# Optimization experiments

Hardware: AMD Instinct MI355X
Metric: run time of the kernel (lower is better)

Reference implementation:

```python
import math
import jax, jax.numpy as jnp
import numpy as np

B, S, D, H, DH = 2, 2048, 2048, 16, 128  # batch, seq (= n_ctx), d_model, n_heads, d_head


def _alibi_slopes(n):
    def pow2(m):
        start = 2 ** (-2 ** (-(math.log2(m) - 3)))
        return [start * start ** i for i in range(m)]
    if math.log2(n).is_integer():
        return pow2(n)
    c = 2 ** math.floor(math.log2(n))
    return pow2(c) + _alibi_slopes(2 * c)[0::2][: n - c]


def _alibi_mask(n_heads, q_len, kv_len):
    # faithful to _gen_alibi_mask: causal -inf upper triangle + slope * key_position
    slopes = jnp.asarray(np.array(_alibi_slopes(n_heads), dtype=np.float32))  # [H]
    bias = slopes[:, None, None] * jnp.arange(kv_len, dtype=jnp.float32)[None, None, :]  # [H,1,kv]
    i = jnp.arange(q_len)[:, None]
    j = jnp.arange(kv_len)[None, :]
    causal = jnp.where(j > i, -jnp.inf, 0.0).astype(jnp.float32)  # [q,kv] (q_len == kv_len here)
    return causal[None, :, :] + bias  # [H,q,kv]


def setup_inputs() -> dict:
    key = jax.random.key(0)
    k1, k2, k3, k4, k5 = jax.random.split(key, 5)
    scale = 1.0 / math.sqrt(D)
    return {
        "resid_pre": jax.random.normal(k1, (B, S, D), dtype=jnp.float32),
        "Wq": jax.random.normal(k2, (H * DH, D), dtype=jnp.float32) * scale,
        "Wk": jax.random.normal(k3, (H * DH, D), dtype=jnp.float32) * scale,
        "Wv": jax.random.normal(k4, (H * DH, D), dtype=jnp.float32) * scale,
        "Wo": jax.random.normal(k5, (D, H * DH), dtype=jnp.float32) * scale,
    }


def reference(resid_pre, Wq, Wk, Wv, Wo):
    b, s, d = resid_pre.shape
    # nn.Linear(no bias): y = x @ W^T ; view to [b, s, H, DH]
    q = (resid_pre @ Wq.T).reshape(b, s, H, DH)
    k = (resid_pre @ Wk.T).reshape(b, s, H, DH)
    v = (resid_pre @ Wv.T).reshape(b, s, H, DH)
    # QK^T / sqrt(d_head), clamp, add ALiBi+causal mask
    scores = jnp.einsum('bqhd,bkhd->bhqk', q, k) / math.sqrt(DH)
    scores = jnp.clip(scores, -1024.0, 1024.0)
    scores = scores + _alibi_mask(H, s, s)[None]  # broadcast over batch
    attn = jax.nn.softmax(scores.astype(jnp.float32), axis=-1).astype(q.dtype)
    z = jnp.einsum('bhqk,bkhd->bqhd', attn, v)  # [b,s,H,DH]
    # out_proj.weight [D, H*DH] reshaped to [D, H, DH]; per-head out summed over heads
    out = jnp.einsum('bqhd,ohd->bqo', z, Wo.reshape(d, H, DH))
    return out
```

## Files before the change

### kernel.cpp

```cpp
#include <hip/hip_runtime.h>
#include <hip/hip_bf16.h>

typedef __attribute__((ext_vector_type(4))) float f32x4;
typedef __attribute__((ext_vector_type(8))) short bf16x8;
typedef __attribute__((ext_vector_type(4))) short short4v;

__device__ __forceinline__ short f2bf(float f) {
  union { float f; unsigned u; } x; x.f = f;
  unsigned r = x.u + 0x7fffu + ((x.u >> 16) & 1u);
  return (short)(r >> 16);
}

__device__ __forceinline__ float fexp2(float x) {
#if __has_builtin(__builtin_amdgcn_exp2f)
  return __builtin_amdgcn_exp2f(x);
#else
  return exp2f(x);
#endif
}

#define WAITVM(n) { asm volatile("s_waitcnt vmcnt(" #n ")" ::: "memory"); __builtin_amdgcn_sched_barrier(0); }
#define BARRIER() { __builtin_amdgcn_sched_barrier(0); asm volatile("s_barrier" ::: "memory"); __builtin_amdgcn_sched_barrier(0); }
#define GLD16(g, l) __builtin_amdgcn_global_load_lds((const __attribute__((address_space(1))) void*)(g), (__attribute__((address_space(3))) void*)(l), 16, 0, 0)

#define QSC (0.08838834764831845f * 1.4426950408889634f)

__global__ __launch_bounds__(256) void cast_kernel(const float* __restrict__ in,
                                                   short* __restrict__ out, int n4) {
  int i = blockIdx.x * 256 + threadIdx.x;
  if (i < n4) {
    const float4 v = reinterpret_cast<const float4*>(in)[i];
    short4v s;
    s.x = f2bf(v.x); s.y = f2bf(v.y); s.z = f2bf(v.z); s.w = f2bf(v.w);
    reinterpret_cast<short4v*>(out)[i] = s;
  }
}

__global__ __launch_bounds__(256) void cast_w_kernel(const float* __restrict__ w0,
                                                     const float* __restrict__ w1,
                                                     const float* __restrict__ w2,
                                                     const float* __restrict__ w3,
                                                     short* __restrict__ qkv,
                                                     short* __restrict__ wo) {
  const int y = blockIdx.y;
  const float* in = (y == 0) ? w0 : (y == 1) ? w1 : (y == 2) ? w2 : w3;
  short* out = (y < 3) ? (qkv + (long)y * 4194304) : wo;
  const int i = blockIdx.x * 256 + threadIdx.x;
  const float4 v = reinterpret_cast<const float4*>(in)[i];
  short4v s;
  s.x = f2bf(v.x); s.y = f2bf(v.y); s.z = f2bf(v.z); s.w = f2bf(v.w);
  reinterpret_cast<short4v*>(out)[i] = s;
}

__global__ __launch_bounds__(512, 2) void gemm_qkv8(const short* __restrict__ A,
                                                    const short* __restrict__ W,
                                                    short* __restrict__ Qo,
                                                    short* __restrict__ Ko,
                                                    short* __restrict__ Vt) {
  __shared__ __align__(1024) char lds[131072];
  const int tid  = threadIdx.x;
  const int lane = tid & 63;
  const int w    = tid >> 6;
  const int wm   = w >> 2, wn = w & 3;
  const int l16  = lane & 15, g = lane >> 4;
  const int K    = 2048;

  int id = (int)blockIdx.x;
  id = (id & 7) * 64 + (id >> 3);
  const int mb = id & 31, nb = id >> 5;
  const long m0 = (long)mb * 128, n0 = (long)nb * 384;

  const int srow = lane >> 3;
  const int scol = ((lane & 7) ^ srow) * 8;
  const int csw  = (l16 & 7) << 4;

  f32x4 acc[4][6];
  #pragma unroll
  for (int a = 0; a < 4; a++)
    #pragma unroll
    for (int b = 0; b < 6; b++) acc[a][b] = (f32x4){0.f, 0.f, 0.f, 0.f};

  #define STAGE_A(kt, buf)                                                          \
    {                                                                               \
      const short* s0_ = A + (m0 + w * 16 + srow) * K + (kt) * 64 + scol;           \
      char* d_ = lds + (buf) * 65536 + (w * 16) * 128;                              \
      GLD16(s0_, d_);                                                               \
      GLD16(s0_ + 8LL * K, d_ + 1024);                                              \
    }
  #define STAGE_B(h, kt, buf)                                                       \
    {                                                                               \
      const short* s0_ = W + (n0 + (h) * 128 + w * 16 + srow) * K + (kt) * 64 + scol; \
      char* d_ = lds + (buf) * 65536 + 16384 + (h) * 16384 + (w * 16) * 128;        \
      GLD16(s0_, d_);                                                               \
      GLD16(s0_ + 8LL * K, d_ + 1024);                                              \
    }

  #define RDA(buf, fmL, k) (*reinterpret_cast<const bf16x8*>(                       \
      lds + (buf) * 65536 + ((wm * 64 + (fmL) * 16 + l16) * 128) +                  \
      ((((k) * 64 + g * 16)) ^ csw)))
  #define RDB(buf, h, j, k) (*reinterpret_cast<const bf16x8*>(                      \
      lds + (buf) * 65536 + 16384 + (h) * 16384 +                                   \
      ((wn * 16 + (j) * 64 + l16) * 128) + ((((k) * 64 + g * 16)) ^ csw)))

  STAGE_A(0, 0);
  STAGE_B(0, 0, 0);
  STAGE_B(1, 0, 0);
  STAGE_B(2, 0, 0);
  WAITVM(4);
  BARRIER();

  bf16x8 af[4][2], bfr[2][2];
  for (int kt = 0; kt < 32; ++kt) {
    const int cur = kt & 1, nxt = cur ^ 1;
    const int ks = (kt + 1 < 32) ? (kt + 1) : kt;

    #pragma unroll
    for (int fm = 0; fm < 4; fm++)
      #pragma unroll
      for (int k = 0; k < 2; k++) af[fm][k] = RDA(cur, fm, k);
    #pragma unroll
    for (int j = 0; j < 2; j++)
      #pragma unroll
      for (int k = 0; k < 2; k++) bfr[j][k] = RDB(cur, 0, j, k);
    STAGE_A(ks, nxt);
    STAGE_B(0, ks, nxt);
    WAITVM(6);
    BARRIER();
    __builtin_amdgcn_s_setprio(1);
    #pragma unroll
    for (int fm = 0; fm < 4; fm++)
      #pragma unroll
      for (int j = 0; j < 2; j++)
        #pragma unroll
        for (int k = 0; k < 2; k++)
          acc[fm][j] = __builtin_amdgcn_mfma_f32_16x16x32_bf16(af[fm][k], bfr[j][k], acc[fm][j], 0, 0, 0);
    __builtin_amdgcn_s_setprio(0);
    BARRIER();

    #pragma unroll
    for (int j = 0; j < 2; j++)
      #pragma unroll
      for (int k = 0; k < 2; k++) bfr[j][k] = RDB(cur, 1, j, k);
    STAGE_B(1, ks, nxt);
    WAITVM(6);
    BARRIER();
    __builtin_amdgcn_s_setprio(1);
    #pragma unroll
    for (int fm = 0; fm < 4; fm++)
      #pragma unroll
      for (int j = 0; j < 2; j++)
        #pragma unroll
        for (int k = 0; k < 2; k++)
          acc[fm][2 + j] = __builtin_amdgcn_mfma_f32_16x16x32_bf16(af[fm][k], bfr[j][k], acc[fm][2 + j], 0, 0, 0);
    __builtin_amdgcn_s_setprio(0);
    BARRIER();

    #pragma unroll
    for (int j = 0; j < 2; j++)
      #pragma unroll
      for (int k = 0; k < 2; k++) bfr[j][k] = RDB(cur, 2, j, k);
    STAGE_B(2, ks, nxt);
    WAITVM(4);
    BARRIER();
    __builtin_amdgcn_s_setprio(1);
    #pragma unroll
    for (int fm = 0; fm < 4; fm++)
      #pragma unroll
      for (int j = 0; j < 2; j++)
        #pragma unroll
        for (int k = 0; k < 2; k++)
          acc[fm][4 + j] = __builtin_amdgcn_mfma_f32_16x16x32_bf16(af[fm][k], bfr[j][k], acc[fm][4 + j], 0, 0, 0);
    __builtin_amdgcn_s_setprio(0);
    BARRIER();
  }

  #pragma unroll
  for (int fm = 0; fm < 4; fm++)
    #pragma unroll
    for (int fj = 0; fj < 6; fj++) {
      const long row0 = m0 + wm * 64 + fm * 16 + g * 4;
      const long col  = n0 + fj * 64 + wn * 16 + l16;
      if (col < 2048) {
        #pragma unroll
        for (int i = 0; i < 4; i++) Qo[(row0 + i) * 2048 + col] = f2bf(acc[fm][fj][i] * QSC);
      } else if (col < 4096) {
        #pragma unroll
        for (int i = 0; i < 4; i++) Ko[(row0 + i) * 2048 + (col - 2048)] = f2bf(acc[fm][fj][i]);
      } else {
        const long c2 = col - 4096;
        const long base = (((row0 >> 11) * 16 + (c2 >> 7)) * 128 + (c2 & 127)) * 2048 + (row0 & 2047);
        short4v pk;
        #pragma unroll
        for (int i = 0; i < 4; i++) pk[i] = f2bf(acc[fm][fj][i]);
        *reinterpret_cast<short4v*>(Vt + base) = pk;
      }
    }
  #undef STAGE_A
  #undef STAGE_B
  #undef RDA
  #undef RDB
}

template<typename CT, bool TV>
__global__ __launch_bounds__(256) void gemm_bt(const short* __restrict__ A,
                                               const short* __restrict__ B,
                                               CT* __restrict__ C,
                                               int M, int N, int K) {
  __shared__ short As[128][72];
  __shared__ short Bs[128][72];

  const int tid  = threadIdx.x;
  const int lane = tid & 63;
  const int w    = tid >> 6;
  const int l16  = lane & 15, g = lane >> 4;
  const int wr   = w >> 1, wc = w & 1;
  const long m0  = (long)blockIdx.y * 128;
  const long n0  = (long)blockIdx.x * 128;

  const f32x4 zero4 = {0.f, 0.f, 0.f, 0.f};
  f32x4 acc[4][4];
  #pragma unroll
  for (int a = 0; a < 4; a++)
    #pragma unroll
    for (int b2 = 0; b2 < 4; b2++) acc[a][b2] = zero4;

  const int srow0 = tid >> 3;
  const int scol  = (tid & 7) * 8;

  const int ktiles = K >> 6;
  for (int kt = 0; kt < ktiles; kt++) {
    const int k0 = kt << 6;
    __syncthreads();
    #pragma unroll
    for (int j = 0; j < 4; j++) {
      const int row = j * 32 + srow0;
      *reinterpret_cast<bf16x8*>(&As[row][scol]) =
          *reinterpret_cast<const bf16x8*>(A + (m0 + row) * K + k0 + scol);
      *reinterpret_cast<bf16x8*>(&Bs[row][scol]) =
          *reinterpret_cast<const bf16x8*>(B + (n0 + row) * K + k0 + scol);
    }
    __syncthreads();
    #pragma unroll
    for (int kk = 0; kk < 2; kk++) {
      bf16x8 af[4], bfr[4];
      #pragma unroll
      for (int f = 0; f < 4; f++)
        af[f] = *reinterpret_cast<const bf16x8*>(&As[wr * 64 + f * 16 + l16][kk * 32 + g * 8]);
      #pragma unroll
      for (int f = 0; f < 4; f++)
        bfr[f] = *reinterpret_cast<const bf16x8*>(&Bs[wc * 64 + f * 16 + l16][kk * 32 + g * 8]);
      #pragma unroll
      for (int fm = 0; fm < 4; fm++)
        #pragma unroll
        for (int fn = 0; fn < 4; fn++)
          acc[fm][fn] = __builtin_amdgcn_mfma_f32_16x16x32_bf16(af[fm], bfr[fn], acc[fm][fn], 0, 0, 0);
    }
  }

  #pragma unroll
  for (int fm = 0; fm < 4; fm++)
    #pragma unroll
    for (int fn = 0; fn < 4; fn++) {
      const long row0 = m0 + wr * 64 + fm * 16 + g * 4;
      const long col  = n0 + wc * 64 + fn * 16 + l16;
      if constexpr (TV) {
        const long base = (((row0 >> 11) * 16 + (col >> 7)) * 128 + (col & 127)) * 2048 + (row0 & 2047);
        short4v pk;
        #pragma unroll
        for (int i = 0; i < 4; i++) pk[i] = f2bf(acc[fm][fn][i]);
        *reinterpret_cast<short4v*>(C + base) = pk;
      } else {
        #pragma unroll
        for (int i = 0; i < 4; i++) {
          const float v = acc[fm][fn][i];
          if constexpr (sizeof(CT) == 2) C[(row0 + i) * N + col] = (CT)f2bf(v);
          else                           C[(row0 + i) * N + col] = v;
        }
      }
    }
}

__global__ __launch_bounds__(256, 3) void attn_kernel(const short* __restrict__ Q,
                                                      const short* __restrict__ K,
                                                      const short* __restrict__ Vt,
                                                      short* __restrict__ Z) {
  __shared__ short Ks[64][136];
  __shared__ short Vs[128][72];
  __shared__ short plds[4][16][72];

  const int tid  = threadIdx.x;
  const int lane = tid & 63;
  const int w    = tid >> 6;
  const int l16  = lane & 15, g = lane >> 4;

  const int bh = blockIdx.x;
  const int bx = 31 - (int)blockIdx.y;
  const int b  = bh >> 4, h = bh & 15;
  const int q0 = bx * 64;

  const float LOG2E  = 1.4426950408889634f;
  const float slope2 = exp2f(-0.5f * (float)(h + 1)) * LOG2E;
  const float CLAMP2 = 1477.3197f;

  bf16x8 qf[4];
  {
    const long qoff = ((long)(b * 2048 + q0 + w * 16 + l16)) * 2048 + h * 128;
    #pragma unroll
    for (int c = 0; c < 4; c++)
      qf[c] = *reinterpret_cast<const bf16x8*>(Q + qoff + c * 32 + g * 8);
  }

  const f32x4 zero4 = {0.f, 0.f, 0.f, 0.f};
  f32x4 zacc[8];
  #pragma unroll
  for (int s = 0; s < 8; s++) zacc[s] = zero4;
  float m2[4], li[4];
  #pragma unroll
  for (int i = 0; i < 4; i++) { m2[i] = -3e38f; li[i] = 0.f; }

  float aj[4];
  #pragma unroll
  for (int ni = 0; ni < 4; ni++) aj[ni] = slope2 * (float)(ni * 16 + l16);

  const int krow = tid >> 4, kcol = (tid & 15) * 8;
  const int vrow = tid >> 3, vcol = (tid & 7) * 8;
  const short* Kh = K + ((long)b * 2048) * 2048 + h * 128;
  const short* Vh = Vt + ((long)(b * 16 + h) * 128) * 2048;

  bf16x8 kreg[4], vreg[4];
  #pragma unroll
  for (int j = 0; j < 4; j++)
    kreg[j] = *reinterpret_cast<const bf16x8*>(Kh + (long)(j * 16 + krow) * 2048 + kcol);
  #pragma unroll
  for (int j = 0; j < 4; j++)
    vreg[j] = *reinterpret_cast<const bf16x8*>(Vh + (long)(j * 32 + vrow) * 2048 + vcol);

  const int ntiles = bx + 1;
  for (int t = 0; t < ntiles; t++) {
    const int kv0 = t * 64;
    __syncthreads();
    #pragma unroll
    for (int j = 0; j < 4; j++)
      *reinterpret_cast<bf16x8*>(&Ks[j * 16 + krow][kcol]) = kreg[j];
    #pragma unroll
    for (int j = 0; j < 4; j++)
      *reinterpret_cast<bf16x8*>(&Vs[j * 32 + vrow][vcol]) = vreg[j];
    __syncthreads();

    f32x4 sc[4];
    #pragma unroll
    for (int ni = 0; ni < 4; ni++) sc[ni] = zero4;
    #pragma unroll
    for (int ni = 0; ni < 4; ni++)
      #pragma unroll
      for (int kc = 0; kc < 4; kc++) {
        const bf16x8 kf = *reinterpret_cast<const bf16x8*>(&Ks[ni * 16 + l16][kc * 32 + g * 8]);
        sc[ni] = __builtin_amdgcn_mfma_f32_16x16x32_bf16(qf[kc], kf, sc[ni], 0, 0, 0);
      }

    if (t + 1 < ntiles) {
      const short* kb = Kh + (long)(kv0 + 64) * 2048;
      const short* vb = Vh + kv0 + 64;
      #pragma unroll
      for (int j = 0; j < 4; j++)
        kreg[j] = *reinterpret_cast<const bf16x8*>(kb + (long)(j * 16 + krow) * 2048 + kcol);
      #pragma unroll
      for (int j = 0; j < 4; j++)
        vreg[j] = *reinterpret_cast<const bf16x8*>(vb + (long)(j * 32 + vrow) * 2048 + vcol);
    }

    const float bk = slope2 * (float)kv0;
    float bn[4];
    #pragma unroll
    for (int ni = 0; ni < 4; ni++) bn[ni] = bk + aj[ni];
    float rmax[4];
    float slack = -3e38f;
    #pragma unroll
    for (int i = 0; i < 4; i++) {
      const int qi = q0 + w * 16 + g * 4 + i;
      float mx = -3e38f;
      #pragma unroll
      for (int ni = 0; ni < 4; ni++) {
        const int j = kv0 + ni * 16 + l16;
        float v = fminf(fmaxf(sc[ni][i], -CLAMP2), CLAMP2) + bn[ni];
        v = (j <= qi) ? v : -3e38f;
        sc[ni][i] = v;
        mx = fmaxf(mx, v);
      }
      rmax[i] = mx;
      slack = fmaxf(slack, mx - m2[i]);
    }
    if (__any(slack > 10.f)) {
      #pragma unroll
      for (int i = 0; i < 4; i++) {
        float bb = rmax[i];
        #pragma unroll
        for (int ms = 1; ms < 16; ms <<= 1) bb = fmaxf(bb, __shfl_xor(bb, ms));
        const float mnew = fmaxf(m2[i], bb);
        const float corr = fexp2(m2[i] - mnew);
        m2[i] = mnew;
        li[i] *= corr;
        #pragma unroll
        for (int s = 0; s < 8; s++) zacc[s][i] *= corr;
      }
    }
    #pragma unroll
    for (int i = 0; i < 4; i++) {
      float psum = 0.f;
      #pragma unroll
      for (int ni = 0; ni < 4; ni++) {
        const float p = fexp2(sc[ni][i] - m2[i]);
        plds[w][g * 4 + i][ni * 16 + l16] = f2bf(p);
        psum += p;
      }
      li[i] += psum;
    }

    bf16x8 paf[2];
    #pragma unroll
    for (int kk = 0; kk < 2; kk++)
      paf[kk] = *reinterpret_cast<const bf16x8*>(&plds[w][l16][kk * 32 + g * 8]);
    #pragma unroll
    for (int s = 0; s < 8; s++) {
      const bf16x8 vf0 = *reinterpret_cast<const bf16x8*>(&Vs[s * 16 + l16][g * 8]);
      const bf16x8 vf1 = *reinterpret_cast<const bf16x8*>(&Vs[s * 16 + l16][32 + g * 8]);
      zacc[s] = __builtin_amdgcn_mfma_f32_16x16x32_bf16(paf[0], vf0, zacc[s], 0, 0, 0);
      zacc[s] = __builtin_amdgcn_mfma_f32_16x16x32_bf16(paf[1], vf1, zacc[s], 0, 0, 0);
    }
  }

  #pragma unroll
  for (int i = 0; i < 4; i++) {
    float s = li[i];
    #pragma unroll
    for (int ms = 1; ms < 16; ms <<= 1) s += __shfl_xor(s, ms);
    li[i] = s;
  }
  #pragma unroll
  for (int s = 0; s < 8; s++)
    #pragma unroll
    for (int i = 0; i < 4; i++) {
      const int qi = q0 + w * 16 + g * 4 + i;
      const float zv = zacc[s][i] / li[i];
      Z[((long)(b * 2048 + qi)) * 2048 + h * 128 + s * 16 + l16] = f2bf(zv);
    }
}

extern "C" void kernel_launch(void* const* d_in, const int* in_sizes, int n_in,
                              void* d_out, int out_size, void* d_ws, size_t ws_size,
                              hipStream_t stream) {
  const float* X  = (const float*)d_in[0];
  const float* Wq = (const float*)d_in[1];
  const float* Wk = (const float*)d_in[2];
  const float* Wv = (const float*)d_in[3];
  const float* Wo = (const float*)d_in[4];
  float* out = (float*)d_out;

  short* ws    = (short*)d_ws;
  short* Xb    = ws;
  short* Wqkvb = ws + 8388608;
  short* Wob   = ws + 20971520;
  short* Qb    = ws + 25165824;
  short* Kb    = ws + 33554432;
  short* Vtb   = ws + 41943040;
  short* Zb    = Xb;

  cast_kernel<<<8192, 256, 0, stream>>>(X, Xb, 2097152);
  dim3 gw(4096, 4);
  cast_w_kernel<<<gw, 256, 0, stream>>>(Wq, Wk, Wv, Wo, Wqkvb, Wob);

  gemm_qkv8<<<512, 512, 0, stream>>>(Xb, Wqkvb, Qb, Kb, Vtb);

  dim3 ga(32, 32);
  attn_kernel<<<ga, 256, 0, stream>>>(Qb, Kb, Vtb, Zb);

  dim3 gg(16, 32);
  gemm_bt<float, false><<<gg, 256, 0, stream>>>(Zb, Wob, out, 4096, 2048, 2048);
}
```

Before: 249.0 us.

## Double attention query tile per block and pipeline output projection GEMM

```diff
diff --git a/kernel.cpp b/kernel.cpp
--- a/kernel.cpp
+++ b/kernel.cpp
@@ -201,92 +201,128 @@
   #undef RDB
 }
 
-template<typename CT, bool TV>
-__global__ __launch_bounds__(256) void gemm_bt(const short* __restrict__ A,
-                                               const short* __restrict__ B,
-                                               CT* __restrict__ C,
-                                               int M, int N, int K) {
-  __shared__ short As[128][72];
-  __shared__ short Bs[128][72];
-
+__global__ __launch_bounds__(512, 2) void gemm_o2(const short* __restrict__ A,
+                                                  const short* __restrict__ W,
+                                                  float* __restrict__ C) {
+  __shared__ __align__(1024) char lds[98304];
   const int tid  = threadIdx.x;
   const int lane = tid & 63;
   const int w    = tid >> 6;
+  const int wm   = w >> 2, wn = w & 3;
   const int l16  = lane & 15, g = lane >> 4;
-  const int wr   = w >> 1, wc = w & 1;
-  const long m0  = (long)blockIdx.y * 128;
-  const long n0  = (long)blockIdx.x * 128;
-
-  const f32x4 zero4 = {0.f, 0.f, 0.f, 0.f};
+  const int K    = 2048;
+
+  int id = (int)blockIdx.x;
+  id = (id & 7) * 32 + (id >> 3);
+  const int mb = id & 31, nb = id >> 5;
+  const long m0 = (long)mb * 128, n0 = (long)nb * 256;
+
+  const int srow = lane >> 3;
+  const int scol = ((lane & 7) ^ srow) * 8;
+  const int csw  = (l16 & 7) << 4;
+
   f32x4 acc[4][4];
   #pragma unroll
   for (int a = 0; a < 4; a++)
     #pragma unroll
-    for (int b2 = 0; b2 < 4; b2++) acc[a][b2] = zero4;
-
-  const int srow0 = tid >> 3;
-  const int scol  = (tid & 7) * 8;
-
-  const int ktiles = K >> 6;
-  for (int kt = 0; kt < ktiles; kt++) {
-    const int k0 = kt << 6;
-    __syncthreads();
-    #pragma unroll
-    for (int j = 0; j < 4; j++) {
-      const int row = j * 32 + srow0;
-      *reinterpret_cast<bf16x8*>(&As[row][scol]) =
-          *reinterpret_cast<const bf16x8*>(A + (m0 + row) * K + k0 + scol);
-      *reinterpret_cast<bf16x8*>(&Bs[row][scol]) =
-          *reinterpret_cast<const bf16x8*>(B + (n0 + row) * K + k0 + scol);
-    }
-    __syncthreads();
-    #pragma unroll
-    for (int kk = 0; kk < 2; kk++) {
-      bf16x8 af[4], bfr[4];
-      #pragma unroll
-      for (int f = 0; f < 4; f++)
-        af[f] = *reinterpret_cast<const bf16x8*>(&As[wr * 64 + f * 16 + l16][kk * 32 + g * 8]);
-      #pragma unroll
-      for (int f = 0; f < 4; f++)
-        bfr[f] = *reinterpret_cast<const bf16x8*>(&Bs[wc * 64 + f * 16 + l16][kk * 32 + g * 8]);
-      #pragma unroll
-      for (int fm = 0; fm < 4; fm++)
-        #pragma unroll
-        for (int fn = 0; fn < 4; fn++)
-          acc[fm][fn] = __builtin_amdgcn_mfma_f32_16x16x32_bf16(af[fm], bfr[fn], acc[fm][fn], 0, 0, 0);
-    }
+    for (int b = 0; b < 4; b++) acc[a][b] = (f32x4){0.f, 0.f, 0.f, 0.f};
+
+  #define OSTAGE_A(kt, buf)                                                         \
+    {                                                                               \
+      const short* s0_ = A + (m0 + w * 16 + srow) * K + (kt) * 64 + scol;           \
+      char* d_ = lds + (buf) * 49152 + (w * 16) * 128;                              \
+      GLD16(s0_, d_);                                                               \
+      GLD16(s0_ + 8LL * K, d_ + 1024);                                              \
+    }
+  #define OSTAGE_B(h, kt, buf)                                                      \
+    {                                                                               \
+      const short* s0_ = W + (n0 + (h) * 128 + w * 16 + srow) * K + (kt) * 64 + scol; \
+      char* d_ = lds + (buf) * 49152 + 16384 + (h) * 16384 + (w * 16) * 128;        \
+      GLD16(s0_, d_);                                                               \
+      GLD16(s0_ + 8LL * K, d_ + 1024);                                              \
+    }
+  #define ORDA(buf, fmL, k) (*reinterpret_cast<const bf16x8*>(                      \
+      lds + (buf) * 49152 + ((wm * 64 + (fmL) * 16 + l16) * 128) +                  \
+      ((((k) * 64 + g * 16)) ^ csw)))
+  #define ORDB(buf, h, j, k) (*reinterpret_cast<const bf16x8*>(                     \
+      lds + (buf) * 49152 + 16384 + (h) * 16384 +                                   \
+      ((wn * 16 + (j) * 64 + l16) * 128) + ((((k) * 64 + g * 16)) ^ csw)))
+
+  OSTAGE_A(0, 0);
+  OSTAGE_B(0, 0, 0);
+  OSTAGE_B(1, 0, 0);
+  WAITVM(2);
+  BARRIER();
+
+  bf16x8 af[4][2], bfr[2][2];
+  for (int kt = 0; kt < 32; ++kt) {
+    const int cur = kt & 1, nxt = cur ^ 1;
+    const int ks = (kt + 1 < 32) ? (kt + 1) : kt;
+
+    #pragma unroll
+    for (int fm = 0; fm < 4; fm++)
+      #pragma unroll
+      for (int k = 0; k < 2; k++) af[fm][k] = ORDA(cur, fm, k);
+    #pragma unroll
+    for (int j = 0; j < 2; j++)
+      #pragma unroll
+      for (int k = 0; k < 2; k++) bfr[j][k] = ORDB(cur, 0, j, k);
+    OSTAGE_A(ks, nxt);
+    OSTAGE_B(0, ks, nxt);
+    WAITVM(4);
+    BARRIER();
+    __builtin_amdgcn_s_setprio(1);
+    #pragma unroll
+    for (int fm = 0; fm < 4; fm++)
+      #pragma unroll
+      for (int j = 0; j < 2; j++)
+        #pragma unroll
+        for (int k = 0; k < 2; k++)
+          acc[fm][j] = __builtin_amdgcn_mfma_f32_16x16x32_bf16(af[fm][k], bfr[j][k], acc[fm][j], 0, 0, 0);
+    __builtin_amdgcn_s_setprio(0);
+    BARRIER();
+
+    #pragma unroll
+    for (int j = 0; j < 2; j++)
+      #pragma unroll
+      for (int k = 0; k < 2; k++) bfr[j][k] = ORDB(cur, 1, j, k);
+    OSTAGE_B(1, ks, nxt);
+    WAITVM(2);
+    BARRIER();
+    __builtin_amdgcn_s_setprio(1);
+    #pragma unroll
+    for (int fm = 0; fm < 4; fm++)
+      #pragma unroll
+      for (int j = 0; j < 2; j++)
+        #pragma unroll
+        for (int k = 0; k < 2; k++)
+          acc[fm][2 + j] = __builtin_amdgcn_mfma_f32_16x16x32_bf16(af[fm][k], bfr[j][k], acc[fm][2 + j], 0, 0, 0);
+    __builtin_amdgcn_s_setprio(0);
+    BARRIER();
   }
 
   #pragma unroll
   for (int fm = 0; fm < 4; fm++)
     #pragma unroll
     for (int fn = 0; fn < 4; fn++) {
-      const long row0 = m0 + wr * 64 + fm * 16 + g * 4;
-      const long col  = n0 + wc * 64 + fn * 16 + l16;
-      if constexpr (TV) {
-        const long base = (((row0 >> 11) * 16 + (col >> 7)) * 128 + (col & 127)) * 2048 + (row0 & 2047);
-        short4v pk;
-        #pragma unroll
-        for (int i = 0; i < 4; i++) pk[i] = f2bf(acc[fm][fn][i]);
-        *reinterpret_cast<short4v*>(C + base) = pk;
-      } else {
-        #pragma unroll
-        for (int i = 0; i < 4; i++) {
-          const float v = acc[fm][fn][i];
-          if constexpr (sizeof(CT) == 2) C[(row0 + i) * N + col] = (CT)f2bf(v);
-          else                           C[(row0 + i) * N + col] = v;
-        }
-      }
-    }
-}
-
-__global__ __launch_bounds__(256, 3) void attn_kernel(const short* __restrict__ Q,
+      const long row0 = m0 + wm * 64 + fm * 16 + g * 4;
+      const long col  = n0 + (fn >> 1) * 128 + (fn & 1) * 64 + wn * 16 + l16;
+      #pragma unroll
+      for (int i = 0; i < 4; i++) C[(row0 + i) * 2048 + col] = acc[fm][fn][i];
+    }
+  #undef OSTAGE_A
+  #undef OSTAGE_B
+  #undef ORDA
+  #undef ORDB
+}
+
+__global__ __launch_bounds__(256, 2) void attn_kernel(const short* __restrict__ Q,
                                                       const short* __restrict__ K,
                                                       const short* __restrict__ Vt,
                                                       short* __restrict__ Z) {
   __shared__ short Ks[64][136];
   __shared__ short Vs[128][72];
-  __shared__ short plds[4][16][72];
+  __shared__ short plds[4][32][72];
 
   const int tid  = threadIdx.x;
   const int lane = tid & 63;
@@ -294,29 +330,34 @@
   const int l16  = lane & 15, g = lane >> 4;
 
   const int bh = blockIdx.x;
-  const int bx = 31 - (int)blockIdx.y;
+  const int bx = 15 - (int)blockIdx.y;
   const int b  = bh >> 4, h = bh & 15;
-  const int q0 = bx * 64;
+  const int q0 = bx * 128;
 
   const float LOG2E  = 1.4426950408889634f;
   const float slope2 = exp2f(-0.5f * (float)(h + 1)) * LOG2E;
   const float CLAMP2 = 1477.3197f;
 
-  bf16x8 qf[4];
-  {
-    const long qoff = ((long)(b * 2048 + q0 + w * 16 + l16)) * 2048 + h * 128;
+  bf16x8 qf[2][4];
+  #pragma unroll
+  for (int mi = 0; mi < 2; mi++) {
+    const long qoff = ((long)(b * 2048 + q0 + w * 32 + mi * 16 + l16)) * 2048 + h * 128;
     #pragma unroll
     for (int c = 0; c < 4; c++)
-      qf[c] = *reinterpret_cast<const bf16x8*>(Q + qoff + c * 32 + g * 8);
+      qf[mi][c] = *reinterpret_cast<const bf16x8*>(Q + qoff + c * 32 + g * 8);
   }
 
   const f32x4 zero4 = {0.f, 0.f, 0.f, 0.f};
-  f32x4 zacc[8];
-  #pragma unroll
-  for (int s = 0; s < 8; s++) zacc[s] = zero4;
-  float m2[4], li[4];
-  #pragma unroll
-  for (int i = 0; i < 4; i++) { m2[i] = -3e38f; li[i] = 0.f; }
+  f32x4 zacc[2][8];
+  #pragma unroll
+  for (int mi = 0; mi < 2; mi++)
+    #pragma unroll
+    for (int s = 0; s < 8; s++) zacc[mi][s] = zero4;
+  float m2[2][4], li[2][4];
+  #pragma unroll
+  for (int mi = 0; mi < 2; mi++)
+    #pragma unroll
+    for (int i = 0; i < 4; i++) { m2[mi][i] = -3e38f; li[mi][i] = 0.f; }
 
   float aj[4];
   #pragma unroll
@@ -335,7 +376,7 @@
   for (int j = 0; j < 4; j++)
     vreg[j] = *reinterpret_cast<const bf16x8*>(Vh + (long)(j * 32 + vrow) * 2048 + vcol);
 
-  const int ntiles = bx + 1;
+  const int ntiles = 2 * bx + 2;
   for (int t = 0; t < ntiles; t++) {
     const int kv0 = t * 64;
     __syncthreads();
@@ -347,16 +388,23 @@
       *reinterpret_cast<bf16x8*>(&Vs[j * 32 + vrow][vcol]) = vreg[j];
     __syncthreads();
 
-    f32x4 sc[4];
-    #pragma unroll
-    for (int ni = 0; ni < 4; ni++) sc[ni] = zero4;
-    #pragma unroll
-    for (int ni = 0; ni < 4; ni++)
-      #pragma unroll
-      for (int kc = 0; kc < 4; kc++) {
-        const bf16x8 kf = *reinterpret_cast<const bf16x8*>(&Ks[ni * 16 + l16][kc * 32 + g * 8]);
-        sc[ni] = __builtin_amdgcn_mfma_f32_16x16x32_bf16(qf[kc], kf, sc[ni], 0, 0, 0);
-      }
+    const bool active = (q0 + w * 32 + 31) >= kv0;
+    f32x4 sc[2][4];
+    if (active) {
+      #pragma unroll
+      for (int mi = 0; mi < 2; mi++)
+        #pragma unroll
+        for (int ni = 0; ni < 4; ni++) sc[mi][ni] = zero4;
+      #pragma unroll
+      for (int ni = 0; ni < 4; ni++)
+        #pragma unroll
+        for (int kc = 0; kc < 4; kc++) {
+          const bf16x8 kf = *reinterpret_cast<const bf16x8*>(&Ks[ni * 16 + l16][kc * 32 + g * 8]);
+          #pragma unroll
+          for (int mi = 0; mi < 2; mi++)
+            sc[mi][ni] = __builtin_amdgcn_mfma_f32_16x16x32_bf16(qf[mi][kc], kf, sc[mi][ni], 0, 0, 0);
+        }
+    }
 
     if (t + 1 < ntiles) {
       const short* kb = Kh + (long)(kv0 + 64) * 2048;
@@ -369,81 +417,98 @@
         vreg[j] = *reinterpret_cast<const bf16x8*>(vb + (long)(j * 32 + vrow) * 2048 + vcol);
     }
 
-    const float bk = slope2 * (float)kv0;
-    float bn[4];
-    #pragma unroll
-    for (int ni = 0; ni < 4; ni++) bn[ni] = bk + aj[ni];
-    float rmax[4];
-    float slack = -3e38f;
+    if (active) {
+      const float bk = slope2 * (float)kv0;
+      float bn[4];
+      #pragma unroll
+      for (int ni = 0; ni < 4; ni++) bn[ni] = bk + aj[ni];
+      float rmax[2][4];
+      float slack = -3e38f;
+      #pragma unroll
+      for (int mi = 0; mi < 2; mi++)
+        #pragma unroll
+        for (int i = 0; i < 4; i++) {
+          const int qi = q0 + w * 32 + mi * 16 + g * 4 + i;
+          float mx = -3e38f;
+          #pragma unroll
+          for (int ni = 0; ni < 4; ni++) {
+            const int j = kv0 + ni * 16 + l16;
+            float v = fminf(fmaxf(sc[mi][ni][i], -CLAMP2), CLAMP2) + bn[ni];
+            v = (j <= qi) ? v : -3e38f;
+            sc[mi][ni][i] = v;
+            mx = fmaxf(mx, v);
+          }
+          rmax[mi][i] = mx;
+          slack = fmaxf(slack, mx - m2[mi][i]);
+        }
+      if (__any(slack > 10.f)) {
+        #pragma unroll
+        for (int mi = 0; mi < 2; mi++)
+          #pragma unroll
+          for (int i = 0; i < 4; i++) {
+            float bb = rmax[mi][i];
+            #pragma unroll
+            for (int ms = 1; ms < 16; ms <<= 1) bb = fmaxf(bb, __shfl_xor(bb, ms));
+            const float mnew = fmaxf(m2[mi][i], bb);
+            const float corr = fexp2(m2[mi][i] - mnew);
+            m2[mi][i] = mnew;
+            li[mi][i] *= corr;
+            #pragma unroll
+            for (int s = 0; s < 8; s++) zacc[mi][s][i] *= corr;
+          }
+      }
+      #pragma unroll
+      for (int mi = 0; mi < 2; mi++)
+        #pragma unroll
+        for (int i = 0; i < 4; i++) {
+          float psum = 0.f;
+          #pragma unroll
+          for (int ni = 0; ni < 4; ni++) {
+            const float p = fexp2(sc[mi][ni][i] - m2[mi][i]);
+            plds[w][mi * 16 + g * 4 + i][ni * 16 + l16] = f2bf(p);
+            psum += p;
+          }
+          li[mi][i] += psum;
+        }
+
+      bf16x8 paf[2][2];
+      #pragma unroll
+      for (int mi = 0; mi < 2; mi++)
+        #pragma unroll
+        for (int kk = 0; kk < 2; kk++)
+          paf[mi][kk] = *reinterpret_cast<const bf16x8*>(&plds[w][mi * 16 + l16][kk * 32 + g * 8]);
+      #pragma unroll
+      for (int s = 0; s < 8; s++) {
+        const bf16x8 vf0 = *reinterpret_cast<const bf16x8*>(&Vs[s * 16 + l16][g * 8]);
+        const bf16x8 vf1 = *reinterpret_cast<const bf16x8*>(&Vs[s * 16 + l16][32 + g * 8]);
+        #pragma unroll
+        for (int mi = 0; mi < 2; mi++) {
+          zacc[mi][s] = __builtin_amdgcn_mfma_f32_16x16x32_bf16(paf[mi][0], vf0, zacc[mi][s], 0, 0, 0);
+          zacc[mi][s] = __builtin_amdgcn_mfma_f32_16x16x32_bf16(paf[mi][1], vf1, zacc[mi][s], 0, 0, 0);
+        }
+      }
+    }
+  }
+
+  #pragma unroll
+  for (int mi = 0; mi < 2; mi++)
     #pragma unroll
     for (int i = 0; i < 4; i++) {
-      const int qi = q0 + w * 16 + g * 4 + i;
-      float mx = -3e38f;
-      #pragma unroll
-      for (int ni = 0; ni < 4; ni++) {
-        const int j = kv0 + ni * 16 + l16;
-        float v = fminf(fmaxf(sc[ni][i], -CLAMP2), CLAMP2) + bn[ni];
-        v = (j <= qi) ? v : -3e38f;
-        sc[ni][i] = v;
-        mx = fmaxf(mx, v);
+      float s = li[mi][i];
+      #pragma unroll
+      for (int ms = 1; ms < 16; ms <<= 1) s += __shfl_xor(s, ms);
+      li[mi][i] = s;
+    }
+  #pragma unroll
+  for (int mi = 0; mi < 2; mi++)
+    #pragma unroll
+    for (int s = 0; s < 8; s++)
+      #pragma unroll
+      for (int i = 0; i < 4; i++) {
+        const int qi = q0 + w * 32 + mi * 16 + g * 4 + i;
+        const float zv = zacc[mi][s][i] / li[mi][i];
+        Z[((long)(b * 2048 + qi)) * 2048 + h * 128 + s * 16 + l16] = f2bf(zv);
       }
-      rmax[i] = mx;
-      slack = fmaxf(slack, mx - m2[i]);
-    }
-    if (__any(slack > 10.f)) {
-      #pragma unroll
-      for (int i = 0; i < 4; i++) {
-        float bb = rmax[i];
-        #pragma unroll
-        for (int ms = 1; ms < 16; ms <<= 1) bb = fmaxf(bb, __shfl_xor(bb, ms));
-        const float mnew = fmaxf(m2[i], bb);
-        const float corr = fexp2(m2[i] - mnew);
-        m2[i] = mnew;
-        li[i] *= corr;
-        #pragma unroll
-        for (int s = 0; s < 8; s++) zacc[s][i] *= corr;
-      }
-    }
-    #pragma unroll
-    for (int i = 0; i < 4; i++) {
-      float psum = 0.f;
-      #pragma unroll
-      for (int ni = 0; ni < 4; ni++) {
-        const float p = fexp2(sc[ni][i] - m2[i]);
-        plds[w][g * 4 + i][ni * 16 + l16] = f2bf(p);
-        psum += p;
-      }
-      li[i] += psum;
-    }
-
-    bf16x8 paf[2];
-    #pragma unroll
-    for (int kk = 0; kk < 2; kk++)
-      paf[kk] = *reinterpret_cast<const bf16x8*>(&plds[w][l16][kk * 32 + g * 8]);
-    #pragma unroll
-    for (int s = 0; s < 8; s++) {
-      const bf16x8 vf0 = *reinterpret_cast<const bf16x8*>(&Vs[s * 16 + l16][g * 8]);
-      const bf16x8 vf1 = *reinterpret_cast<const bf16x8*>(&Vs[s * 16 + l16][32 + g * 8]);
-      zacc[s] = __builtin_amdgcn_mfma_f32_16x16x32_bf16(paf[0], vf0, zacc[s], 0, 0, 0);
-      zacc[s] = __builtin_amdgcn_mfma_f32_16x16x32_bf16(paf[1], vf1, zacc[s], 0, 0, 0);
-    }
-  }
-
-  #pragma unroll
-  for (int i = 0; i < 4; i++) {
-    float s = li[i];
-    #pragma unroll
-    for (int ms = 1; ms < 16; ms <<= 1) s += __shfl_xor(s, ms);
-    li[i] = s;
-  }
-  #pragma unroll
-  for (int s = 0; s < 8; s++)
-    #pragma unroll
-    for (int i = 0; i < 4; i++) {
-      const int qi = q0 + w * 16 + g * 4 + i;
-      const float zv = zacc[s][i] / li[i];
-      Z[((long)(b * 2048 + qi)) * 2048 + h * 128 + s * 16 + l16] = f2bf(zv);
-    }
 }
 
 extern "C" void kernel_launch(void* const* d_in, const int* in_sizes, int n_in,
@@ -471,9 +536,8 @@
 
   gemm_qkv8<<<512, 512, 0, stream>>>(Xb, Wqkvb, Qb, Kb, Vtb);
 
-  dim3 ga(32, 32);
+  dim3 ga(32, 16);
   attn_kernel<<<ga, 256, 0, stream>>>(Qb, Kb, Vtb, Zb);
 
-  dim3 gg(16, 32);
-  gemm_bt<float, false><<<gg, 256, 0, stream>>>(Zb, Wob, out, 4096, 2048, 2048);
-}
+  gemm_o2<<<256, 512, 0, stream>>>(Zb, Wob, out);
+}
```

Measured after the change: 263.9 us. 6.0% more time.
